# Kernel optimization log

Hardware: AMD Instinct MI355X
Metric: run time of the kernel (lower is better)

Reference implementation:

```python
import jax, jax.numpy as jnp
import numpy as np

NUM_HEADS = 16
NUM_FEATURES = 1024
HEAD_DIM = NUM_FEATURES // NUM_HEADS
MAX_WAVELENGTH = 10000.0
SCALE_FACTOR = 1.0


def apply_rope(x, positions):
    # x: [B, S, H, D], positions: [B, S]
    half = HEAD_DIM // 2
    fraction = 2.0 * jnp.arange(half, dtype=x.dtype) / HEAD_DIM
    timescale = MAX_WAVELENGTH ** fraction                      # [half]
    sinusoid = positions[..., None].astype(x.dtype) / timescale  # [B, S, half]
    sinusoid = sinusoid[..., None, :] / SCALE_FACTOR             # [B, S, 1, half]
    sin, cos = jnp.sin(sinusoid), jnp.cos(sinusoid)
    x1, x2 = jnp.split(x, 2, axis=-1)
    return jnp.concatenate([x1 * cos - x2 * sin, x2 * cos + x1 * sin], axis=-1).astype(x.dtype)


def setup_inputs() -> dict:
    key = jax.random.key(0)
    ks = jax.random.split(key, 9)
    B, S, F = 2, 2048, NUM_FEATURES
    std = 1.0 / np.sqrt(F)
    inp = {
        "x": jax.random.normal(ks[0], (B, S, F), dtype=jnp.float32),
        "positions": jnp.broadcast_to(jnp.arange(S, dtype=jnp.int32), (B, S)),
        "Wq": jax.random.normal(ks[1], (F, F), dtype=jnp.float32) * std,
        "bq": jnp.zeros((F,), dtype=jnp.float32),
        "Wk": jax.random.normal(ks[2], (F, F), dtype=jnp.float32) * std,
        "bk": jnp.zeros((F,), dtype=jnp.float32),
        "Wv": jax.random.normal(ks[3], (F, F), dtype=jnp.float32) * std,
        "bv": jnp.zeros((F,), dtype=jnp.float32),
        "Wo": jax.random.normal(ks[4], (F, F), dtype=jnp.float32) * std,
        "bo": jnp.zeros((F,), dtype=jnp.float32),
    }
    return inp


def reference(x, positions, Wq, bq, Wk, bk, Wv, bv, Wo, bo):
    B, S, F = x.shape
    H, D = NUM_HEADS, HEAD_DIM
    q = (x @ Wq + bq).reshape(B, S, H, D)
    k = (x @ Wk + bk).reshape(B, S, H, D)
    v = (x @ Wv + bv).reshape(B, S, H, D)
    q = apply_rope(q, positions)
    k = apply_rope(k, positions)
    scale = jnp.sqrt(jnp.asarray(D, dtype=x.dtype))
    # scores: [B, H, S, S]
    scores = jnp.einsum("bqhd,bkhd->bhqk", q, k) / scale
    causal = jnp.tril(jnp.ones((S, S), dtype=bool))
    big_neg = jnp.finfo(scores.dtype).min
    scores = jnp.where(causal, scores, big_neg)
    attn = jax.nn.softmax(scores, axis=-1)
    out = jnp.einsum("bhqk,bkhd->bqhd", attn, v).reshape(B, S, F)
    return out @ Wo + bo
```

## Files before the change

### kernel.cpp

```cpp
#include <hip/hip_runtime.h>
#include <hip/hip_bf16.h>

#define S_LEN 2048
#define NF 1024
#define NH 16
#define HD 64
#define NB 2
#define M_TOT 4096

typedef __bf16 bf16x8 __attribute__((ext_vector_type(8)));
typedef float f32x4 __attribute__((ext_vector_type(4)));
typedef unsigned short u16;

__device__ __forceinline__ u16 f2bf(float f) {
  union { float f; unsigned u; } v; v.f = f;
  unsigned r = v.u + 0x7FFFu + ((v.u >> 16) & 1u);
  return (u16)(r >> 16);
}

__device__ __forceinline__ unsigned pk2bf(float a, float b) {
  __hip_bfloat162 t = __float22bfloat162_rn(make_float2(a, b));
  union { __hip_bfloat162 h; unsigned u; } u; u.h = t; return u.u;
}

__device__ __forceinline__ f32x4 mfma16(bf16x8 a, bf16x8 b, f32x4 c) {
  return __builtin_amdgcn_mfma_f32_16x16x32_bf16(a, b, c, 0, 0, 0);
}

__device__ __forceinline__ void gll16(const u16* g, u16* l) {
  __builtin_amdgcn_global_load_lds(
      (const __attribute__((address_space(1))) unsigned int*)g,
      (__attribute__((address_space(3))) unsigned int*)l, 16, 0, 0);
}

__device__ __forceinline__ u16* swz(u16* base, int row, int chunk) {
  return (u16*)((char*)base + row * 128 + ((chunk ^ (row & 7)) * 16));
}
__device__ __forceinline__ const u16* swz(const u16* base, int row, int chunk) {
  return (const u16*)((const char*)base + row * 128 + ((chunk ^ (row & 7)) * 16));
}

__global__ void __launch_bounds__(256) cast_kernel(const float* __restrict__ in,
                                                   u16* __restrict__ out) {
  int i = (blockIdx.x * 256 + threadIdx.x) * 4;
  float4 v = *(const float4*)(in + i);
  ushort4 o;
  o.x = f2bf(v.x); o.y = f2bf(v.y); o.z = f2bf(v.z); o.w = f2bf(v.w);
  *(ushort4*)(out + i) = o;
}

__global__ void __launch_bounds__(256) rope_table_kernel(const int* __restrict__ positions,
                                                         float2* __restrict__ tab) {
  int idx = blockIdx.x * 256 + threadIdx.x;
  int p = idx & 31;
  int bs = idx >> 5;
  float pos = (float)positions[bs];
  float ang = pos / __powf(10000.0f, (float)p * (1.0f / 32.0f));
  float sn, cs;
  sincosf(ang, &sn, &cs);
  tab[idx] = make_float2(sn, cs);
}

__global__ void __launch_bounds__(256) wtrans_kernel(
    const float* __restrict__ W0, const float* __restrict__ W1,
    const float* __restrict__ W2, const float* __restrict__ W3,
    u16* __restrict__ T0, u16* __restrict__ T1,
    u16* __restrict__ T2, u16* __restrict__ T3) {
  const float* W = (blockIdx.z == 0) ? W0 : (blockIdx.z == 1) ? W1 : (blockIdx.z == 2) ? W2 : W3;
  u16* Wt = (blockIdx.z == 0) ? T0 : (blockIdx.z == 1) ? T1 : (blockIdx.z == 2) ? T2 : T3;
  __shared__ float t[32][33];
  int n0 = blockIdx.x * 32, k0 = blockIdx.y * 32;
  int tx = threadIdx.x, ty0 = threadIdx.y;
#pragma unroll
  for (int i = 0; i < 4; i++) {
    int ty = ty0 + i * 8;
    t[ty][tx] = W[(size_t)(k0 + ty) * NF + n0 + tx];
  }
  __syncthreads();
#pragma unroll
  for (int i = 0; i < 4; i++) {
    int ty = ty0 + i * 8;
    Wt[(size_t)(n0 + ty) * NF + k0 + tx] = f2bf(t[tx][ty]);
  }
}

__device__ __forceinline__ void mm_core(const u16* __restrict__ A, const u16* __restrict__ Bt,
                                        int m0, int n0, u16* As, u16* Bs, f32x4 acc[4][4]) {
  const int tid = threadIdx.x;
  const int lane = tid & 63, w = tid >> 6;
  const int l15 = lane & 15, quad = lane >> 4;
  const int wr = w >> 1, wc = w & 1;
#pragma unroll
  for (int i = 0; i < 4; i++)
#pragma unroll
    for (int j = 0; j < 4; j++) {
      f32x4 z = {0.f, 0.f, 0.f, 0.f};
      acc[i][j] = z;
    }
  for (int k0 = 0; k0 < NF; k0 += 32) {
    __syncthreads();
#pragma unroll
    for (int i = 0; i < 2; i++) {
      int ci = (w * 2 + i) * 64 + lane;
      int row = ci >> 2, c = ci & 3;
      gll16(&A[(size_t)(m0 + row) * NF + k0 + c * 8], &As[(w * 2 + i) * 512]);
      gll16(&Bt[(size_t)(n0 + row) * NF + k0 + c * 8], &Bs[(w * 2 + i) * 512]);
    }
    __syncthreads();
    bf16x8 af[4], bfr[4];
#pragma unroll
    for (int i = 0; i < 4; i++)
      af[i] = *(const bf16x8*)&As[(wr * 64 + i * 16 + l15) * 32 + quad * 8];
#pragma unroll
    for (int j = 0; j < 4; j++)
      bfr[j] = *(const bf16x8*)&Bs[(wc * 64 + j * 16 + l15) * 32 + quad * 8];
#pragma unroll
    for (int i = 0; i < 4; i++)
#pragma unroll
      for (int j = 0; j < 4; j++)
        acc[i][j] = mfma16(af[i], bfr[j], acc[i][j]);
  }
}

#define QSCL 0.18033688f

__global__ void __launch_bounds__(256) gemm_qkv_kernel(
    const u16* __restrict__ xb,
    const u16* __restrict__ wtq, const u16* __restrict__ wtk, const u16* __restrict__ wtv,
    const float* __restrict__ bq, const float* __restrict__ bk, const float* __restrict__ bv,
    const float2* __restrict__ rtab,
    u16* __restrict__ qo, u16* __restrict__ ko, u16* __restrict__ vto) {
  __shared__ u16 As[128 * 32], Bs[128 * 32];
  const int z = blockIdx.z;
  const u16* Wt = (z == 0) ? wtq : (z == 1) ? wtk : wtv;
  const float* bias = (z == 0) ? bq : (z == 1) ? bk : bv;
  const int m0 = blockIdx.y * 128, n0 = blockIdx.x * 128;
  f32x4 acc[4][4];
  mm_core(xb, Wt, m0, n0, As, Bs, acc);
  const int tid = threadIdx.x;
  const int lane = tid & 63, w = tid >> 6;
  const int l15 = lane & 15, quad = lane >> 4;
  const int wr = w >> 1, wc = w & 1;
  if (z < 2) {
    u16* out = (z == 0) ? qo : ko;
    const float oscl = (z == 0) ? QSCL : 1.0f;
#pragma unroll
    for (int i = 0; i < 4; i++) {
#pragma unroll
      for (int r = 0; r < 4; r++) {
        int gm = m0 + wr * 64 + i * 16 + quad * 4 + r;
        int b = gm >> 11, s = gm & 2047;
#pragma unroll
        for (int j = 0; j < 2; j++) {
          int col1 = n0 + wc * 64 + j * 16 + l15;
          int p = j * 16 + l15;
          float2 sc = rtab[gm * 32 + p];
          float x1 = acc[i][j][r] + bias[col1];
          float x2 = acc[i][j + 2][r] + bias[col1 + 32];
          float o1 = (x1 * sc.y - x2 * sc.x) * oscl;
          float o2 = (x2 * sc.y + x1 * sc.x) * oscl;
          int h = col1 >> 6;
          size_t base = ((size_t)((b * NH + h) * S_LEN + s)) * HD;
          out[base + p] = f2bf(o1);
          out[base + p + 32] = f2bf(o2);
        }
      }
    }
  } else {
#pragma unroll
    for (int i = 0; i < 4; i++) {
      int gm0 = m0 + wr * 64 + i * 16 + quad * 4;
      int b = gm0 >> 11, s0 = gm0 & 2047;
#pragma unroll
      for (int j = 0; j < 4; j++) {
        int col = n0 + wc * 64 + j * 16 + l15;
        int h = col >> 6, d = col & 63;
        float bb = bias[col];
        ushort4 pk;
        pk.x = f2bf(acc[i][j][0] + bb);
        pk.y = f2bf(acc[i][j][1] + bb);
        pk.z = f2bf(acc[i][j][2] + bb);
        pk.w = f2bf(acc[i][j][3] + bb);
        *(ushort4*)&vto[((size_t)((b * NH + h) * HD + d)) * S_LEN + s0] = pk;
      }
    }
  }
}

__global__ void __launch_bounds__(256) gemm_o_kernel(const u16* __restrict__ ab,
                                                     const u16* __restrict__ wto,
                                                     const float* __restrict__ bo,
                                                     float* __restrict__ out) {
  __shared__ u16 As[128 * 32], Bs[128 * 32];
  const int m0 = blockIdx.y * 128, n0 = blockIdx.x * 128;
  f32x4 acc[4][4];
  mm_core(ab, wto, m0, n0, As, Bs, acc);
  const int tid = threadIdx.x;
  const int lane = tid & 63, w = tid >> 6;
  const int l15 = lane & 15, quad = lane >> 4;
  const int wr = w >> 1, wc = w & 1;
#pragma unroll
  for (int i = 0; i < 4; i++) {
#pragma unroll
    for (int j = 0; j < 4; j++) {
      int col = n0 + wc * 64 + j * 16 + l15;
      float bb = bo[col];
#pragma unroll
      for (int r = 0; r < 4; r++) {
        int gm = m0 + wr * 64 + i * 16 + quad * 4 + r;
        out[(size_t)gm * NF + col] = acc[i][j][r] + bb;
      }
    }
  }
}

__global__ void __launch_bounds__(256) attn_kernel(const u16* __restrict__ qb,
                                                   const u16* __restrict__ kb,
                                                   const u16* __restrict__ vtb,
                                                   u16* __restrict__ ob) {
  __shared__ u16 ks[2][64 * 64];
  __shared__ u16 vs[2][64 * 64];
  __shared__ u16 ps[4][32 * 64];
  const int bx = blockIdx.x;
  const int qt = (bx < 256) ? (15 - (bx >> 5)) : ((bx - 256) >> 5);
  const int bh = bx & 31;
  const int tid = threadIdx.x;
  const int lane = tid & 63, w = tid >> 6, l15 = lane & 15, quad = lane >> 4;
  const int bb = bh >> 4, h = bh & 15;
  const size_t kvbase = (size_t)bh * S_LEN;
  const size_t vbase = (size_t)bh * HD;
  const int Q0 = qt * 128;
  const int nit = 2 * (qt + 1);
  const int r0 = tid >> 3, c0 = tid & 7;
  const int r1 = r0 + 32;

  bf16x8 qf[2][2];
#pragma unroll
  for (int c = 0; c < 2; c++) {
    const u16* qrow = &qb[(kvbase + Q0 + w * 32 + c * 16 + l15) * HD];
#pragma unroll
    for (int hh = 0; hh < 2; hh++)
      qf[c][hh] = *(const bf16x8*)&qrow[hh * 32 + quad * 8];
  }

  float mrun[2] = {-1e30f, -1e30f}, lrun[2] = {0.f, 0.f};
  f32x4 Oa[2][4];
#pragma unroll
  for (int g = 0; g < 2; g++)
#pragma unroll
    for (int t = 0; t < 4; t++) { f32x4 z = {0.f, 0.f, 0.f, 0.f}; Oa[g][t] = z; }

  *(uint4*)swz(ks[0], r0, c0) = *(const uint4*)&kb[(kvbase + r0) * HD + c0 * 8];
  *(uint4*)swz(ks[0], r1, c0) = *(const uint4*)&kb[(kvbase + r1) * HD + c0 * 8];
  *(uint4*)swz(vs[0], r0, c0) = *(const uint4*)&vtb[(vbase + r0) * S_LEN + c0 * 8];
  *(uint4*)swz(vs[0], r1, c0) = *(const uint4*)&vtb[(vbase + r1) * S_LEN + c0 * 8];
  __syncthreads();

  for (int it = 0; it < nit; ++it) {
    const int bsel = it & 1;
    const int k0 = it * 64;
    uint4 pk0, pk1, pv0, pv1;
    const bool pf = (it + 1 < nit);
    if (pf) {
      int k1 = k0 + 64;
      pk0 = *(const uint4*)&kb[(kvbase + k1 + r0) * HD + c0 * 8];
      pk1 = *(const uint4*)&kb[(kvbase + k1 + r1) * HD + c0 * 8];
      pv0 = *(const uint4*)&vtb[(vbase + r0) * S_LEN + k1 + c0 * 8];
      pv1 = *(const uint4*)&vtb[(vbase + r1) * S_LEN + k1 + c0 * 8];
    }
    f32x4 sf[2][4];
#pragma unroll
    for (int t = 0; t < 4; t++) {
      bf16x8 ak0 = *(const bf16x8*)swz(ks[bsel], t * 16 + l15, quad);
      bf16x8 ak1 = *(const bf16x8*)swz(ks[bsel], t * 16 + l15, 4 + quad);
#pragma unroll
      for (int c = 0; c < 2; c++) {
        f32x4 z = {0.f, 0.f, 0.f, 0.f};
        z = mfma16(ak0, qf[c][0], z);
        z = mfma16(ak1, qf[c][1], z);
        sf[c][t] = z;
      }
    }
    if (it >= 2 * qt) {
#pragma unroll
      for (int c = 0; c < 2; c++) {
        int qg = Q0 + w * 32 + c * 16 + l15;
#pragma unroll
        for (int t = 0; t < 4; t++)
#pragma unroll
          for (int r = 0; r < 4; r++)
            if (k0 + t * 16 + quad * 4 + r > qg) sf[c][t][r] = -1e30f;
      }
    }
    float alph[2];
#pragma unroll
    for (int c = 0; c < 2; c++) {
      float mx = sf[c][0][0];
#pragma unroll
      for (int t = 0; t < 4; t++)
#pragma unroll
        for (int r = 0; r < 4; r++) mx = fmaxf(mx, sf[c][t][r]);
      mx = fmaxf(mx, __shfl_xor(mx, 16, 64));
      mx = fmaxf(mx, __shfl_xor(mx, 32, 64));
      float mnew = fmaxf(mrun[c], mx);
      float al = __builtin_amdgcn_exp2f(mrun[c] - mnew);
      float rs = 0.f;
#pragma unroll
      for (int t = 0; t < 4; t++)
#pragma unroll
        for (int r = 0; r < 4; r++) {
          float e = __builtin_amdgcn_exp2f(sf[c][t][r] - mnew);
          sf[c][t][r] = e;
          rs += e;
        }
      rs += __shfl_xor(rs, 16, 64);
      rs += __shfl_xor(rs, 32, 64);
      lrun[c] = al * lrun[c] + rs;
      mrun[c] = mnew;
      alph[c] = al;
    }
    if (__any((alph[0] < 1.f) || (alph[1] < 1.f))) {
#pragma unroll
      for (int g = 0; g < 2; g++)
#pragma unroll
        for (int r = 0; r < 4; r++) {
          float ao = __shfl(alph[g], quad * 4 + r, 64);
#pragma unroll
          for (int t = 0; t < 4; t++) Oa[g][t][r] *= ao;
        }
    }
#pragma unroll
    for (int c = 0; c < 2; c++) {
      int row = c * 16 + l15;
#pragma unroll
      for (int t = 0; t < 4; t++) {
        uint2 pk;
        pk.x = pk2bf(sf[c][t][0], sf[c][t][1]);
        pk.y = pk2bf(sf[c][t][2], sf[c][t][3]);
        int chnk = 2 * t + (quad >> 1);
        *(uint2*)((char*)ps[w] + row * 128 + ((chnk ^ (row & 7)) * 16) + (quad & 1) * 8) = pk;
      }
    }
    __builtin_amdgcn_wave_barrier();
    bf16x8 ap[2][2];
#pragma unroll
    for (int g = 0; g < 2; g++)
#pragma unroll
      for (int hh = 0; hh < 2; hh++)
        ap[g][hh] = *(const bf16x8*)swz(ps[w], g * 16 + l15, hh * 4 + quad);
#pragma unroll
    for (int t = 0; t < 4; t++) {
      bf16x8 bv0 = *(const bf16x8*)swz(vs[bsel], t * 16 + l15, quad);
      bf16x8 bv1 = *(const bf16x8*)swz(vs[bsel], t * 16 + l15, 4 + quad);
#pragma unroll
      for (int g = 0; g < 2; g++) {
        Oa[g][t] = mfma16(ap[g][0], bv0, Oa[g][t]);
        Oa[g][t] = mfma16(ap[g][1], bv1, Oa[g][t]);
      }
    }
    if (pf) {
      *(uint4*)swz(ks[bsel ^ 1], r0, c0) = pk0;
      *(uint4*)swz(ks[bsel ^ 1], r1, c0) = pk1;
      *(uint4*)swz(vs[bsel ^ 1], r0, c0) = pv0;
      *(uint4*)swz(vs[bsel ^ 1], r1, c0) = pv1;
    }
    __syncthreads();
  }
#pragma unroll
  for (int g = 0; g < 2; g++) {
#pragma unroll
    for (int r = 0; r < 4; r++) {
      float lr = __shfl(lrun[g], quad * 4 + r, 64);
      float inv = 1.f / lr;
      int qg = Q0 + w * 32 + g * 16 + quad * 4 + r;
      size_t rowb = ((size_t)(bb * S_LEN + qg)) * NF + h * HD;
#pragma unroll
      for (int t = 0; t < 4; t++)
        ob[rowb + t * 16 + l15] = f2bf(Oa[g][t][r] * inv);
    }
  }
}

extern "C" void kernel_launch(void* const* d_in, const int* in_sizes, int n_in,
                              void* d_out, int out_size, void* d_ws, size_t ws_size,
                              hipStream_t stream) {
  const float* x  = (const float*)d_in[0];
  const int* pos  = (const int*)d_in[1];
  const float* Wq = (const float*)d_in[2];
  const float* bq = (const float*)d_in[3];
  const float* Wk = (const float*)d_in[4];
  const float* bk = (const float*)d_in[5];
  const float* Wv = (const float*)d_in[6];
  const float* bv = (const float*)d_in[7];
  const float* Wo = (const float*)d_in[8];
  const float* bo = (const float*)d_in[9];
  float* out = (float*)d_out;

  u16* xb  = (u16*)d_ws;
  u16* wtq = xb + (size_t)M_TOT * NF;
  u16* wtk = wtq + (size_t)NF * NF;
  u16* wtv = wtk + (size_t)NF * NF;
  u16* wto = wtv + (size_t)NF * NF;
  u16* qb  = wto + (size_t)NF * NF;
  u16* kb  = qb + (size_t)M_TOT * NF;
  u16* vtb = kb + (size_t)M_TOT * NF;
  float2* rtab = (float2*)(vtb + (size_t)M_TOT * NF);
  u16* attnb = xb;

  cast_kernel<<<dim3(M_TOT * NF / 1024), 256, 0, stream>>>(x, xb);
  rope_table_kernel<<<dim3(NB * S_LEN * 32 / 256), 256, 0, stream>>>(pos, rtab);
  wtrans_kernel<<<dim3(32, 32, 4), dim3(32, 8), 0, stream>>>(Wq, Wk, Wv, Wo,
                                                             wtq, wtk, wtv, wto);
  gemm_qkv_kernel<<<dim3(8, 32, 3), 256, 0, stream>>>(xb, wtq, wtk, wtv, bq, bk, bv,
                                                      rtab, qb, kb, vtb);
  attn_kernel<<<dim3(512), 256, 0, stream>>>(qb, kb, vtb, attnb);
  gemm_o_kernel<<<dim3(8, 32), 256, 0, stream>>>(attnb, wto, bo, out);
}
```

Measured before the change: 231.1 us.

## Split long causal attention tiles across blocks with atomic-counter partial merge

Replaces the one-block-per-query-tile attention with a split-KV scheme: query tiles with more key blocks are divided into up to four chunks, each handled by its own block, giving 1280 blocks with more even work. Partial O, max and row-sum are written to workspace, and the last finishing block (found via an atomic counter) merges them. The row-sum is now computed with MFMA against a ones vector instead of shuffles, and K/V staging drops from double to single buffering with two barriers per iteration to allow higher occupancy. This adds fp32 partial traffic, a memset launch, and extra synchronisation.

Result: slower. 615.3 us (+166.3%).

```diff
diff --git a/kernel.cpp b/kernel.cpp
--- a/kernel.cpp
+++ b/kernel.cpp
@@ -7,6 +7,7 @@
 #define HD 64
 #define NB 2
 #define M_TOT 4096
+#define NCHUNK_TOT 1280
 
 typedef __bf16 bf16x8 __attribute__((ext_vector_type(8)));
 typedef float f32x4 __attribute__((ext_vector_type(4)));
@@ -39,6 +40,14 @@
 __device__ __forceinline__ const u16* swz(const u16* base, int row, int chunk) {
   return (const u16*)((const char*)base + row * 128 + ((chunk ^ (row & 7)) * 16));
 }
+
+__device__ const signed char QT_OF[40] = {0,1,2,3, 4,4, 5,5, 6,6, 7,7,
+                                          8,8,8, 9,9,9, 10,10,10, 11,11,11,
+                                          12,12,12,12, 13,13,13,13,
+                                          14,14,14,14, 15,15,15,15};
+__device__ const signed char CI_OF[40] = {0,0,0,0, 0,1, 0,1, 0,1, 0,1,
+                                          0,1,2, 0,1,2, 0,1,2, 0,1,2,
+                                          0,1,2,3, 0,1,2,3, 0,1,2,3, 0,1,2,3};
 
 __global__ void __launch_bounds__(256) cast_kernel(const float* __restrict__ in,
                                                    u16* __restrict__ out) {
@@ -214,26 +223,34 @@
   }
 }
 
-__global__ void __launch_bounds__(256) attn_kernel(const u16* __restrict__ qb,
-                                                   const u16* __restrict__ kb,
-                                                   const u16* __restrict__ vtb,
-                                                   u16* __restrict__ ob) {
-  __shared__ u16 ks[2][64 * 64];
-  __shared__ u16 vs[2][64 * 64];
+__global__ void __launch_bounds__(256, 4) attn_kernel(
+    const u16* __restrict__ qb, const u16* __restrict__ kb,
+    const u16* __restrict__ vtb, u16* __restrict__ ob,
+    float* __restrict__ partO, float* __restrict__ partM,
+    float* __restrict__ partL, int* __restrict__ cnt) {
+  __shared__ u16 ks[64 * 64];
+  __shared__ u16 vs[64 * 64];
   __shared__ u16 ps[4][32 * 64];
+  __shared__ int s_old;
   const int bx = blockIdx.x;
-  const int qt = (bx < 256) ? (15 - (bx >> 5)) : ((bx - 256) >> 5);
-  const int bh = bx & 31;
+  const int bh = bx / 40, r40 = bx - bh * 40;
+  const int qt = QT_OF[r40], ci = CI_OF[r40];
+  const int nch = (qt >> 2) + 1;
+  const int T = 2 * (qt + 1);
+  const int t0 = ci * T / nch, t1 = (ci + 1) * T / nch;
   const int tid = threadIdx.x;
   const int lane = tid & 63, w = tid >> 6, l15 = lane & 15, quad = lane >> 4;
   const int bb = bh >> 4, h = bh & 15;
   const size_t kvbase = (size_t)bh * S_LEN;
   const size_t vbase = (size_t)bh * HD;
   const int Q0 = qt * 128;
-  const int nit = 2 * (qt + 1);
   const int r0 = tid >> 3, c0 = tid & 7;
   const int r1 = r0 + 32;
 
+  bf16x8 ones;
+#pragma unroll
+  for (int i = 0; i < 8; i++) ones[i] = (__bf16)1.0f;
+
   bf16x8 qf[2][2];
 #pragma unroll
   for (int c = 0; c < 2; c++) {
@@ -243,24 +260,29 @@
       qf[c][hh] = *(const bf16x8*)&qrow[hh * 32 + quad * 8];
   }
 
-  float mrun[2] = {-1e30f, -1e30f}, lrun[2] = {0.f, 0.f};
-  f32x4 Oa[2][4];
-#pragma unroll
-  for (int g = 0; g < 2; g++)
-#pragma unroll
-    for (int t = 0; t < 4; t++) { f32x4 z = {0.f, 0.f, 0.f, 0.f}; Oa[g][t] = z; }
-
-  *(uint4*)swz(ks[0], r0, c0) = *(const uint4*)&kb[(kvbase + r0) * HD + c0 * 8];
-  *(uint4*)swz(ks[0], r1, c0) = *(const uint4*)&kb[(kvbase + r1) * HD + c0 * 8];
-  *(uint4*)swz(vs[0], r0, c0) = *(const uint4*)&vtb[(vbase + r0) * S_LEN + c0 * 8];
-  *(uint4*)swz(vs[0], r1, c0) = *(const uint4*)&vtb[(vbase + r1) * S_LEN + c0 * 8];
+  float mrun[2] = {-1e30f, -1e30f};
+  f32x4 Oa[2][4], lacc[2];
+#pragma unroll
+  for (int g = 0; g < 2; g++) {
+    f32x4 z = {0.f, 0.f, 0.f, 0.f};
+    lacc[g] = z;
+#pragma unroll
+    for (int t = 0; t < 4; t++) Oa[g][t] = z;
+  }
+
+  {
+    int kk = t0 * 64;
+    *(uint4*)swz(ks, r0, c0) = *(const uint4*)&kb[(kvbase + kk + r0) * HD + c0 * 8];
+    *(uint4*)swz(ks, r1, c0) = *(const uint4*)&kb[(kvbase + kk + r1) * HD + c0 * 8];
+    *(uint4*)swz(vs, r0, c0) = *(const uint4*)&vtb[(vbase + r0) * S_LEN + kk + c0 * 8];
+    *(uint4*)swz(vs, r1, c0) = *(const uint4*)&vtb[(vbase + r1) * S_LEN + kk + c0 * 8];
+  }
   __syncthreads();
 
-  for (int it = 0; it < nit; ++it) {
-    const int bsel = it & 1;
+  for (int it = t0; it < t1; ++it) {
     const int k0 = it * 64;
+    const bool pf = (it + 1 < t1);
     uint4 pk0, pk1, pv0, pv1;
-    const bool pf = (it + 1 < nit);
     if (pf) {
       int k1 = k0 + 64;
       pk0 = *(const uint4*)&kb[(kvbase + k1 + r0) * HD + c0 * 8];
@@ -271,8 +293,8 @@
     f32x4 sf[2][4];
 #pragma unroll
     for (int t = 0; t < 4; t++) {
-      bf16x8 ak0 = *(const bf16x8*)swz(ks[bsel], t * 16 + l15, quad);
-      bf16x8 ak1 = *(const bf16x8*)swz(ks[bsel], t * 16 + l15, 4 + quad);
+      bf16x8 ak0 = *(const bf16x8*)swz(ks, t * 16 + l15, quad);
+      bf16x8 ak1 = *(const bf16x8*)swz(ks, t * 16 + l15, 4 + quad);
 #pragma unroll
       for (int c = 0; c < 2; c++) {
         f32x4 z = {0.f, 0.f, 0.f, 0.f};
@@ -288,8 +310,8 @@
 #pragma unroll
         for (int t = 0; t < 4; t++)
 #pragma unroll
-          for (int r = 0; r < 4; r++)
-            if (k0 + t * 16 + quad * 4 + r > qg) sf[c][t][r] = -1e30f;
+          for (int rr = 0; rr < 4; rr++)
+            if (k0 + t * 16 + quad * 4 + rr > qg) sf[c][t][rr] = -1e30f;
       }
     }
     float alph[2];
@@ -299,34 +321,27 @@
 #pragma unroll
       for (int t = 0; t < 4; t++)
 #pragma unroll
-        for (int r = 0; r < 4; r++) mx = fmaxf(mx, sf[c][t][r]);
+        for (int rr = 0; rr < 4; rr++) mx = fmaxf(mx, sf[c][t][rr]);
       mx = fmaxf(mx, __shfl_xor(mx, 16, 64));
       mx = fmaxf(mx, __shfl_xor(mx, 32, 64));
       float mnew = fmaxf(mrun[c], mx);
-      float al = __builtin_amdgcn_exp2f(mrun[c] - mnew);
-      float rs = 0.f;
+      alph[c] = __builtin_amdgcn_exp2f(mrun[c] - mnew);
+      mrun[c] = mnew;
 #pragma unroll
       for (int t = 0; t < 4; t++)
 #pragma unroll
-        for (int r = 0; r < 4; r++) {
-          float e = __builtin_amdgcn_exp2f(sf[c][t][r] - mnew);
-          sf[c][t][r] = e;
-          rs += e;
-        }
-      rs += __shfl_xor(rs, 16, 64);
-      rs += __shfl_xor(rs, 32, 64);
-      lrun[c] = al * lrun[c] + rs;
-      mrun[c] = mnew;
-      alph[c] = al;
+        for (int rr = 0; rr < 4; rr++)
+          sf[c][t][rr] = __builtin_amdgcn_exp2f(sf[c][t][rr] - mnew);
     }
     if (__any((alph[0] < 1.f) || (alph[1] < 1.f))) {
 #pragma unroll
       for (int g = 0; g < 2; g++)
 #pragma unroll
-        for (int r = 0; r < 4; r++) {
-          float ao = __shfl(alph[g], quad * 4 + r, 64);
-#pragma unroll
-          for (int t = 0; t < 4; t++) Oa[g][t][r] *= ao;
+        for (int rr = 0; rr < 4; rr++) {
+          float ao = __shfl(alph[g], quad * 4 + rr, 64);
+#pragma unroll
+          for (int t = 0; t < 4; t++) Oa[g][t][rr] *= ao;
+          lacc[g][rr] *= ao;
         }
     }
 #pragma unroll
@@ -350,34 +365,87 @@
         ap[g][hh] = *(const bf16x8*)swz(ps[w], g * 16 + l15, hh * 4 + quad);
 #pragma unroll
     for (int t = 0; t < 4; t++) {
-      bf16x8 bv0 = *(const bf16x8*)swz(vs[bsel], t * 16 + l15, quad);
-      bf16x8 bv1 = *(const bf16x8*)swz(vs[bsel], t * 16 + l15, 4 + quad);
+      bf16x8 bv0 = *(const bf16x8*)swz(vs, t * 16 + l15, quad);
+      bf16x8 bv1 = *(const bf16x8*)swz(vs, t * 16 + l15, 4 + quad);
 #pragma unroll
       for (int g = 0; g < 2; g++) {
         Oa[g][t] = mfma16(ap[g][0], bv0, Oa[g][t]);
         Oa[g][t] = mfma16(ap[g][1], bv1, Oa[g][t]);
       }
     }
+#pragma unroll
+    for (int g = 0; g < 2; g++) {
+      lacc[g] = mfma16(ap[g][0], ones, lacc[g]);
+      lacc[g] = mfma16(ap[g][1], ones, lacc[g]);
+    }
     if (pf) {
-      *(uint4*)swz(ks[bsel ^ 1], r0, c0) = pk0;
-      *(uint4*)swz(ks[bsel ^ 1], r1, c0) = pk1;
-      *(uint4*)swz(vs[bsel ^ 1], r0, c0) = pv0;
-      *(uint4*)swz(vs[bsel ^ 1], r1, c0) = pv1;
-    }
-    __syncthreads();
-  }
-#pragma unroll
-  for (int g = 0; g < 2; g++) {
-#pragma unroll
-    for (int r = 0; r < 4; r++) {
-      float lr = __shfl(lrun[g], quad * 4 + r, 64);
-      float inv = 1.f / lr;
-      int qg = Q0 + w * 32 + g * 16 + quad * 4 + r;
-      size_t rowb = ((size_t)(bb * S_LEN + qg)) * NF + h * HD;
+      __syncthreads();
+      *(uint4*)swz(ks, r0, c0) = pk0;
+      *(uint4*)swz(ks, r1, c0) = pk1;
+      *(uint4*)swz(vs, r0, c0) = pv0;
+      *(uint4*)swz(vs, r1, c0) = pv1;
+      __syncthreads();
+    }
+  }
+
+  if (nch == 1) {
+#pragma unroll
+    for (int g = 0; g < 2; g++)
+#pragma unroll
+      for (int rr = 0; rr < 4; rr++) {
+        float inv = 1.f / lacc[g][rr];
+        int qg = Q0 + w * 32 + g * 16 + quad * 4 + rr;
+        size_t rowb = ((size_t)(bb * S_LEN + qg)) * NF + h * HD;
+#pragma unroll
+        for (int t = 0; t < 4; t++)
+          ob[rowb + t * 16 + l15] = f2bf(Oa[g][t][rr] * inv);
+      }
+    return;
+  }
+
+  const int slot = bx;
+  float* po = partO + (size_t)slot * 8192;
+#pragma unroll
+  for (int g = 0; g < 2; g++)
+#pragma unroll
+    for (int rr = 0; rr < 4; rr++) {
+      int ql = w * 32 + g * 16 + quad * 4 + rr;
 #pragma unroll
       for (int t = 0; t < 4; t++)
-        ob[rowb + t * 16 + l15] = f2bf(Oa[g][t][r] * inv);
-    }
+        po[ql * 64 + t * 16 + l15] = Oa[g][t][rr];
+      if (l15 == 0) partL[slot * 128 + ql] = lacc[g][rr];
+    }
+  if (quad == 0) {
+#pragma unroll
+    for (int c = 0; c < 2; c++)
+      partM[slot * 128 + w * 32 + c * 16 + l15] = mrun[c];
+  }
+  __threadfence();
+  __syncthreads();
+  const int tile = bh * 16 + qt;
+  if (tid == 0) s_old = atomicAdd(&cnt[tile], 1);
+  __syncthreads();
+  if (s_old != nch - 1) return;
+  __threadfence();
+
+  const int base = bx - ci;
+  const int d = tid & 63, q4 = tid >> 6;
+  for (int i = 0; i < 32; i++) {
+    int ql = q4 + i * 4;
+    float ms = -1e30f;
+#pragma unroll
+    for (int c = 0; c < 4; c++)
+      if (c < nch) ms = fmaxf(ms, partM[(base + c) * 128 + ql]);
+    float os = 0.f, ls = 0.f;
+#pragma unroll
+    for (int c = 0; c < 4; c++)
+      if (c < nch) {
+        float wgt = __builtin_amdgcn_exp2f(partM[(base + c) * 128 + ql] - ms);
+        os += wgt * partO[(size_t)(base + c) * 8192 + ql * 64 + d];
+        ls += wgt * partL[(base + c) * 128 + ql];
+      }
+    size_t rowb = ((size_t)(bb * S_LEN + Q0 + ql)) * NF + h * HD;
+    ob[rowb + d] = f2bf(os / ls);
   }
 }
 
@@ -405,14 +473,20 @@
   u16* kb  = qb + (size_t)M_TOT * NF;
   u16* vtb = kb + (size_t)M_TOT * NF;
   float2* rtab = (float2*)(vtb + (size_t)M_TOT * NF);
+  float* partO = (float*)(rtab + (size_t)NB * S_LEN * 32);
+  float* partM = partO + (size_t)NCHUNK_TOT * 8192;
+  float* partL = partM + (size_t)NCHUNK_TOT * 128;
+  int* cnt = (int*)(partL + (size_t)NCHUNK_TOT * 128);
   u16* attnb = xb;
 
+  hipMemsetAsync(cnt, 0, 512 * sizeof(int), stream);
   cast_kernel<<<dim3(M_TOT * NF / 1024), 256, 0, stream>>>(x, xb);
   rope_table_kernel<<<dim3(NB * S_LEN * 32 / 256), 256, 0, stream>>>(pos, rtab);
   wtrans_kernel<<<dim3(32, 32, 4), dim3(32, 8), 0, stream>>>(Wq, Wk, Wv, Wo,
                                                              wtq, wtk, wtv, wto);
   gemm_qkv_kernel<<<dim3(8, 32, 3), 256, 0, stream>>>(xb, wtq, wtk, wtv, bq, bk, bv,
                                                       rtab, qb, kb, vtb);
-  attn_kernel<<<dim3(512), 256, 0, stream>>>(qb, kb, vtb, attnb);
+  attn_kernel<<<dim3(NCHUNK_TOT), 256, 0, stream>>>(qb, kb, vtb, attnb,
+                                                    partO, partM, partL, cnt);
   gemm_o_kernel<<<dim3(8, 32), 256, 0, stream>>>(attnb, wto, bo, out);
 }
```

## Process 128-key tiles per iteration and compute row sums via MFMA

Applied to the files above, without the earlier changes.

The attention loop now handles two 64-key subtiles per iteration, halving the trip count and block-wide barriers, though each iteration now uses two barriers and both LDS buffers with no double buffering. The softmax row sum is computed by an MFMA against a ones vector on the bf16 probabilities, replacing the per-lane sum and its cross-lane shuffles. Launch bounds request 4 blocks per CU, which may limit registers. Prefetched registers double, and the normalizer is now taken from rounded bf16 probabilities.

After: 265.9 us. 15.1% more time.

```diff
diff --git a/kernel.cpp b/kernel.cpp
--- a/kernel.cpp
+++ b/kernel.cpp
@@ -214,10 +214,9 @@
   }
 }
 
-__global__ void __launch_bounds__(256) attn_kernel(const u16* __restrict__ qb,
-                                                   const u16* __restrict__ kb,
-                                                   const u16* __restrict__ vtb,
-                                                   u16* __restrict__ ob) {
+__global__ void __launch_bounds__(256, 4) attn_kernel(
+    const u16* __restrict__ qb, const u16* __restrict__ kb,
+    const u16* __restrict__ vtb, u16* __restrict__ ob) {
   __shared__ u16 ks[2][64 * 64];
   __shared__ u16 vs[2][64 * 64];
   __shared__ u16 ps[4][32 * 64];
@@ -230,10 +229,14 @@
   const size_t kvbase = (size_t)bh * S_LEN;
   const size_t vbase = (size_t)bh * HD;
   const int Q0 = qt * 128;
-  const int nit = 2 * (qt + 1);
+  const int nit = qt + 1;
   const int r0 = tid >> 3, c0 = tid & 7;
   const int r1 = r0 + 32;
 
+  bf16x8 ones;
+#pragma unroll
+  for (int i = 0; i < 8; i++) ones[i] = (__bf16)1.0f;
+
   bf16x8 qf[2][2];
 #pragma unroll
   for (int c = 0; c < 2; c++) {
@@ -243,142 +246,155 @@
       qf[c][hh] = *(const bf16x8*)&qrow[hh * 32 + quad * 8];
   }
 
-  float mrun[2] = {-1e30f, -1e30f}, lrun[2] = {0.f, 0.f};
-  f32x4 Oa[2][4];
+  float mrun[2] = {-1e30f, -1e30f};
+  f32x4 Oa[2][4], lacc[2];
+#pragma unroll
+  for (int g = 0; g < 2; g++) {
+    f32x4 z = {0.f, 0.f, 0.f, 0.f};
+    lacc[g] = z;
+#pragma unroll
+    for (int t = 0; t < 4; t++) Oa[g][t] = z;
+  }
+
+#pragma unroll
+  for (int u = 0; u < 2; u++) {
+    *(uint4*)swz(ks[u], r0, c0) = *(const uint4*)&kb[(kvbase + u * 64 + r0) * HD + c0 * 8];
+    *(uint4*)swz(ks[u], r1, c0) = *(const uint4*)&kb[(kvbase + u * 64 + r1) * HD + c0 * 8];
+    *(uint4*)swz(vs[u], r0, c0) = *(const uint4*)&vtb[(vbase + r0) * S_LEN + u * 64 + c0 * 8];
+    *(uint4*)swz(vs[u], r1, c0) = *(const uint4*)&vtb[(vbase + r1) * S_LEN + u * 64 + c0 * 8];
+  }
+  __syncthreads();
+
+  for (int it = 0; it < nit; ++it) {
+    const bool pf = (it + 1 < nit);
+    const bool last = (it == nit - 1);
+    uint4 pk[2][2], pv[2][2];
+    if (pf) {
+      int k1 = (it + 1) * 128;
+#pragma unroll
+      for (int u = 0; u < 2; u++) {
+        pk[u][0] = *(const uint4*)&kb[(kvbase + k1 + u * 64 + r0) * HD + c0 * 8];
+        pk[u][1] = *(const uint4*)&kb[(kvbase + k1 + u * 64 + r1) * HD + c0 * 8];
+        pv[u][0] = *(const uint4*)&vtb[(vbase + r0) * S_LEN + k1 + u * 64 + c0 * 8];
+        pv[u][1] = *(const uint4*)&vtb[(vbase + r1) * S_LEN + k1 + u * 64 + c0 * 8];
+      }
+    }
+#pragma unroll
+    for (int u = 0; u < 2; u++) {
+      const int k0u = it * 128 + u * 64;
+      f32x4 sf[2][4];
+#pragma unroll
+      for (int t = 0; t < 4; t++) {
+        bf16x8 ak0 = *(const bf16x8*)swz(ks[u], t * 16 + l15, quad);
+        bf16x8 ak1 = *(const bf16x8*)swz(ks[u], t * 16 + l15, 4 + quad);
+#pragma unroll
+        for (int c = 0; c < 2; c++) {
+          f32x4 z = {0.f, 0.f, 0.f, 0.f};
+          z = mfma16(ak0, qf[c][0], z);
+          z = mfma16(ak1, qf[c][1], z);
+          sf[c][t] = z;
+        }
+      }
+      if (last) {
+#pragma unroll
+        for (int c = 0; c < 2; c++) {
+          int qg = Q0 + w * 32 + c * 16 + l15;
+#pragma unroll
+          for (int t = 0; t < 4; t++)
+#pragma unroll
+            for (int rr = 0; rr < 4; rr++)
+              if (k0u + t * 16 + quad * 4 + rr > qg) sf[c][t][rr] = -1e30f;
+        }
+      }
+      float alph[2];
+#pragma unroll
+      for (int c = 0; c < 2; c++) {
+        float mx = sf[c][0][0];
+#pragma unroll
+        for (int t = 0; t < 4; t++)
+#pragma unroll
+          for (int rr = 0; rr < 4; rr++) mx = fmaxf(mx, sf[c][t][rr]);
+        mx = fmaxf(mx, __shfl_xor(mx, 16, 64));
+        mx = fmaxf(mx, __shfl_xor(mx, 32, 64));
+        float mnew = fmaxf(mrun[c], mx);
+        alph[c] = __builtin_amdgcn_exp2f(mrun[c] - mnew);
+        mrun[c] = mnew;
+#pragma unroll
+        for (int t = 0; t < 4; t++)
+#pragma unroll
+          for (int rr = 0; rr < 4; rr++)
+            sf[c][t][rr] = __builtin_amdgcn_exp2f(sf[c][t][rr] - mnew);
+      }
+      if (__any((alph[0] < 1.f) || (alph[1] < 1.f))) {
+#pragma unroll
+        for (int g = 0; g < 2; g++)
+#pragma unroll
+          for (int rr = 0; rr < 4; rr++) {
+            float ao = __shfl(alph[g], quad * 4 + rr, 64);
+#pragma unroll
+            for (int t = 0; t < 4; t++) Oa[g][t][rr] *= ao;
+            lacc[g][rr] *= ao;
+          }
+      }
+#pragma unroll
+      for (int c = 0; c < 2; c++) {
+        int row = c * 16 + l15;
+#pragma unroll
+        for (int t = 0; t < 4; t++) {
+          uint2 pkk;
+          pkk.x = pk2bf(sf[c][t][0], sf[c][t][1]);
+          pkk.y = pk2bf(sf[c][t][2], sf[c][t][3]);
+          int chnk = 2 * t + (quad >> 1);
+          *(uint2*)((char*)ps[w] + row * 128 + ((chnk ^ (row & 7)) * 16) + (quad & 1) * 8) = pkk;
+        }
+      }
+      __builtin_amdgcn_wave_barrier();
+      bf16x8 ap[2][2];
+#pragma unroll
+      for (int g = 0; g < 2; g++)
+#pragma unroll
+        for (int hh = 0; hh < 2; hh++)
+          ap[g][hh] = *(const bf16x8*)swz(ps[w], g * 16 + l15, hh * 4 + quad);
+#pragma unroll
+      for (int t = 0; t < 4; t++) {
+        bf16x8 bv0 = *(const bf16x8*)swz(vs[u], t * 16 + l15, quad);
+        bf16x8 bv1 = *(const bf16x8*)swz(vs[u], t * 16 + l15, 4 + quad);
+#pragma unroll
+        for (int g = 0; g < 2; g++) {
+          Oa[g][t] = mfma16(ap[g][0], bv0, Oa[g][t]);
+          Oa[g][t] = mfma16(ap[g][1], bv1, Oa[g][t]);
+        }
+      }
+#pragma unroll
+      for (int g = 0; g < 2; g++) {
+        lacc[g] = mfma16(ap[g][0], ones, lacc[g]);
+        lacc[g] = mfma16(ap[g][1], ones, lacc[g]);
+      }
+    }
+    if (pf) {
+      __syncthreads();
+#pragma unroll
+      for (int u = 0; u < 2; u++) {
+        *(uint4*)swz(ks[u], r0, c0) = pk[u][0];
+        *(uint4*)swz(ks[u], r1, c0) = pk[u][1];
+        *(uint4*)swz(vs[u], r0, c0) = pv[u][0];
+        *(uint4*)swz(vs[u], r1, c0) = pv[u][1];
+      }
+      __syncthreads();
+    }
+  }
+
 #pragma unroll
   for (int g = 0; g < 2; g++)
 #pragma unroll
-    for (int t = 0; t < 4; t++) { f32x4 z = {0.f, 0.f, 0.f, 0.f}; Oa[g][t] = z; }
-
-  *(uint4*)swz(ks[0], r0, c0) = *(const uint4*)&kb[(kvbase + r0) * HD + c0 * 8];
-  *(uint4*)swz(ks[0], r1, c0) = *(const uint4*)&kb[(kvbase + r1) * HD + c0 * 8];
-  *(uint4*)swz(vs[0], r0, c0) = *(const uint4*)&vtb[(vbase + r0) * S_LEN + c0 * 8];
-  *(uint4*)swz(vs[0], r1, c0) = *(const uint4*)&vtb[(vbase + r1) * S_LEN + c0 * 8];
-  __syncthreads();
-
-  for (int it = 0; it < nit; ++it) {
-    const int bsel = it & 1;
-    const int k0 = it * 64;
-    uint4 pk0, pk1, pv0, pv1;
-    const bool pf = (it + 1 < nit);
-    if (pf) {
-      int k1 = k0 + 64;
-      pk0 = *(const uint4*)&kb[(kvbase + k1 + r0) * HD + c0 * 8];
-      pk1 = *(const uint4*)&kb[(kvbase + k1 + r1) * HD + c0 * 8];
-      pv0 = *(const uint4*)&vtb[(vbase + r0) * S_LEN + k1 + c0 * 8];
-      pv1 = *(const uint4*)&vtb[(vbase + r1) * S_LEN + k1 + c0 * 8];
-    }
-    f32x4 sf[2][4];
-#pragma unroll
-    for (int t = 0; t < 4; t++) {
-      bf16x8 ak0 = *(const bf16x8*)swz(ks[bsel], t * 16 + l15, quad);
-      bf16x8 ak1 = *(const bf16x8*)swz(ks[bsel], t * 16 + l15, 4 + quad);
-#pragma unroll
-      for (int c = 0; c < 2; c++) {
-        f32x4 z = {0.f, 0.f, 0.f, 0.f};
-        z = mfma16(ak0, qf[c][0], z);
-        z = mfma16(ak1, qf[c][1], z);
-        sf[c][t] = z;
-      }
-    }
-    if (it >= 2 * qt) {
-#pragma unroll
-      for (int c = 0; c < 2; c++) {
-        int qg = Q0 + w * 32 + c * 16 + l15;
-#pragma unroll
-        for (int t = 0; t < 4; t++)
-#pragma unroll
-          for (int r = 0; r < 4; r++)
-            if (k0 + t * 16 + quad * 4 + r > qg) sf[c][t][r] = -1e30f;
-      }
-    }
-    float alph[2];
-#pragma unroll
-    for (int c = 0; c < 2; c++) {
-      float mx = sf[c][0][0];
+    for (int rr = 0; rr < 4; rr++) {
+      float inv = 1.f / lacc[g][rr];
+      int qg = Q0 + w * 32 + g * 16 + quad * 4 + rr;
+      size_t rowb = ((size_t)(bb * S_LEN + qg)) * NF + h * HD;
 #pragma unroll
       for (int t = 0; t < 4; t++)
-#pragma unroll
-        for (int r = 0; r < 4; r++) mx = fmaxf(mx, sf[c][t][r]);
-      mx = fmaxf(mx, __shfl_xor(mx, 16, 64));
-      mx = fmaxf(mx, __shfl_xor(mx, 32, 64));
-      float mnew = fmaxf(mrun[c], mx);
-      float al = __builtin_amdgcn_exp2f(mrun[c] - mnew);
-      float rs = 0.f;
-#pragma unroll
-      for (int t = 0; t < 4; t++)
-#pragma unroll
-        for (int r = 0; r < 4; r++) {
-          float e = __builtin_amdgcn_exp2f(sf[c][t][r] - mnew);
-          sf[c][t][r] = e;
-          rs += e;
-        }
-      rs += __shfl_xor(rs, 16, 64);
-      rs += __shfl_xor(rs, 32, 64);
-      lrun[c] = al * lrun[c] + rs;
-      mrun[c] = mnew;
-      alph[c] = al;
-    }
-    if (__any((alph[0] < 1.f) || (alph[1] < 1.f))) {
-#pragma unroll
-      for (int g = 0; g < 2; g++)
-#pragma unroll
-        for (int r = 0; r < 4; r++) {
-          float ao = __shfl(alph[g], quad * 4 + r, 64);
-#pragma unroll
-          for (int t = 0; t < 4; t++) Oa[g][t][r] *= ao;
-        }
-    }
-#pragma unroll
-    for (int c = 0; c < 2; c++) {
-      int row = c * 16 + l15;
-#pragma unroll
-      for (int t = 0; t < 4; t++) {
-        uint2 pk;
-        pk.x = pk2bf(sf[c][t][0], sf[c][t][1]);
-        pk.y = pk2bf(sf[c][t][2], sf[c][t][3]);
-        int chnk = 2 * t + (quad >> 1);
-        *(uint2*)((char*)ps[w] + row * 128 + ((chnk ^ (row & 7)) * 16) + (quad & 1) * 8) = pk;
-      }
-    }
-    __builtin_amdgcn_wave_barrier();
-    bf16x8 ap[2][2];
-#pragma unroll
-    for (int g = 0; g < 2; g++)
-#pragma unroll
-      for (int hh = 0; hh < 2; hh++)
-        ap[g][hh] = *(const bf16x8*)swz(ps[w], g * 16 + l15, hh * 4 + quad);
-#pragma unroll
-    for (int t = 0; t < 4; t++) {
-      bf16x8 bv0 = *(const bf16x8*)swz(vs[bsel], t * 16 + l15, quad);
-      bf16x8 bv1 = *(const bf16x8*)swz(vs[bsel], t * 16 + l15, 4 + quad);
-#pragma unroll
-      for (int g = 0; g < 2; g++) {
-        Oa[g][t] = mfma16(ap[g][0], bv0, Oa[g][t]);
-        Oa[g][t] = mfma16(ap[g][1], bv1, Oa[g][t]);
-      }
-    }
-    if (pf) {
-      *(uint4*)swz(ks[bsel ^ 1], r0, c0) = pk0;
-      *(uint4*)swz(ks[bsel ^ 1], r1, c0) = pk1;
-      *(uint4*)swz(vs[bsel ^ 1], r0, c0) = pv0;
-      *(uint4*)swz(vs[bsel ^ 1], r1, c0) = pv1;
-    }
-    __syncthreads();
-  }
-#pragma unroll
-  for (int g = 0; g < 2; g++) {
-#pragma unroll
-    for (int r = 0; r < 4; r++) {
-      float lr = __shfl(lrun[g], quad * 4 + r, 64);
-      float inv = 1.f / lr;
-      int qg = Q0 + w * 32 + g * 16 + quad * 4 + r;
-      size_t rowb = ((size_t)(bb * S_LEN + qg)) * NF + h * HD;
-#pragma unroll
-      for (int t = 0; t < 4; t++)
-        ob[rowb + t * 16 + l15] = f2bf(Oa[g][t][r] * inv);
-    }
-  }
+        ob[rowb + t * 16 + l15] = f2bf(Oa[g][t][rr] * inv);
+    }
 }
 
 extern "C" void kernel_launch(void* const* d_in, const int* in_sizes, int n_in,
```
